# Kernel tuning notes

Measured on AMD Instinct MI355X. Metric: run time of the kernel, lower is better.

Reference implementation:

```python
import jax, jax.numpy as jnp
import numpy as np

T, B, D, H = 512, 128, 256, 256
SIGMA = 0.01


def setup_inputs() -> dict:
    key = jax.random.key(0)
    ks = jax.random.split(key, 5)
    inputs = jax.random.normal(ks[0], (T, B, D), dtype=jnp.float32)
    W_xh_f = jax.random.normal(ks[1], (D, H), dtype=jnp.float32) * SIGMA
    W_hh_f = jax.random.normal(ks[2], (H, H), dtype=jnp.float32) * SIGMA
    b_h_f = jnp.zeros((H,), dtype=jnp.float32)
    W_xh_b = jax.random.normal(ks[3], (D, H), dtype=jnp.float32) * SIGMA
    W_hh_b = jax.random.normal(ks[4], (H, H), dtype=jnp.float32) * SIGMA
    b_h_b = jnp.zeros((H,), dtype=jnp.float32)
    return {"inputs": inputs, "W_xh_f": W_xh_f, "W_hh_f": W_hh_f, "b_h_f": b_h_f,
            "W_xh_b": W_xh_b, "W_hh_b": W_hh_b, "b_h_b": b_h_b}


def _rnn(inputs, W_xh, W_hh, b_h):
    # inputs: [T, B, D]; returns outputs [T, B, H], final state [B, H]
    h0 = jnp.zeros((inputs.shape[1], W_hh.shape[0]), dtype=inputs.dtype)
    # Precompute input projections for all steps (one big GEMM).
    xW = jnp.einsum('tbd,dh->tbh', inputs, W_xh) + b_h

    def step(h, xw_t):
        h = jnp.tanh(xw_t + h @ W_hh)
        return h, h

    hT, outs = jax.lax.scan(step, h0, xW)
    return outs, hT


def reference(inputs, W_xh_f, W_hh_f, b_h_f, W_xh_b, W_hh_b, b_h_b):
    f_outs, f_H = _rnn(inputs, W_xh_f, W_hh_f, b_h_f)          # forward direction
    b_outs, b_H = _rnn(inputs[::-1], W_xh_b, W_hh_b, b_h_b)    # backward direction
    # align backward outputs with original time order and concat on feature dim
    outputs = jnp.concatenate([f_outs, b_outs[::-1]], axis=-1)  # [T, B, 2H]
    return outputs, f_H, b_H
```

## Files before the change

kernel.cpp:

```cpp
#include <hip/hip_runtime.h>
#include <hip/hip_bf16.h>
#include <stdint.h>


typedef short sh8   __attribute__((ext_vector_type(8)));
typedef float f32x4 __attribute__((ext_vector_type(4)));

#define TT 512
#define BB 128
#define HH 256
#define LDH 264

__device__ __forceinline__ unsigned short f2bf(float x) {
    union { float f; unsigned u; } v; v.f = x;
    unsigned r = v.u + 0x7FFFu + ((v.u >> 16) & 1u);
    return (unsigned short)(r >> 16);
}
__device__ __forceinline__ unsigned pk2bf(float lo, float hi) {
    union { __hip_bfloat162 b; unsigned u; } c;
    c.b = __float22bfloat162_rn(make_float2(lo, hi));
    return c.u;
}
__device__ __forceinline__ float tanh5(float x) {
    float e = __builtin_amdgcn_exp2f(x * 2.8853900817779268f);
    return __builtin_fmaf(-2.0f, __builtin_amdgcn_rcpf(e + 1.0f), 1.0f);
}
__device__ __forceinline__ void bar_lds() {
    asm volatile("s_waitcnt lgkmcnt(0)\n\ts_barrier" ::: "memory");
}
__device__ __forceinline__ sh8 pack8(float4 a, float4 b) {
    union { sh8 s; unsigned u[4]; } c;
    c.u[0] = pk2bf(a.x, a.y); c.u[1] = pk2bf(a.z, a.w);
    c.u[2] = pk2bf(b.x, b.y); c.u[3] = pk2bf(b.z, b.w);
    return c.s;
}

__global__ __launch_bounds__(512, 2) void xw_precompute(
    const float* __restrict__ x,
    const float* __restrict__ Wxf, const float* __restrict__ bhf,
    const float* __restrict__ Wxb, const float* __restrict__ bhb,
    float* __restrict__ out)
{
    __shared__ __align__(16) unsigned short xb[2][16 * LDH];

    const int tid = threadIdx.x;
    const int w  = tid >> 6, l = tid & 63;
    const int li = l & 15, lq = l >> 4;
    const int N0 = w * 32;
    const int r0 = blockIdx.x * 256;

    sh8 wf[2][2][8];
#pragma unroll
    for (int d = 0; d < 2; ++d) {
        const float* W = d ? Wxb : Wxf;
#pragma unroll
        for (int nt = 0; nt < 2; ++nt)
#pragma unroll
            for (int kf = 0; kf < 8; ++kf) {
                sh8 t;
#pragma unroll
                for (int j = 0; j < 8; ++j)
                    t[j] = (short)f2bf(W[(size_t)(kf * 32 + lq * 8 + j) * HH + N0 + nt * 16 + li]);
                wf[d][nt][kf] = t;
            }
    }
    f32x4 bias4[2][2];
#pragma unroll
    for (int d = 0; d < 2; ++d) {
        const float* bs = d ? bhb : bhf;
#pragma unroll
        for (int nt = 0; nt < 2; ++nt)
            bias4[d][nt] = *(const f32x4*)&bs[N0 + nt * 16 + lq * 4];
    }

    const int sm = tid >> 5;
    const int sk = (tid & 31) * 8;
    const float* xrow = x + (size_t)(r0 + sm) * HH + sk;

    {
        float4 v0 = *(const float4*)xrow;
        float4 v1 = *(const float4*)(xrow + 4);
        *(sh8*)&xb[0][sm * LDH + sk] = pack8(v0, v1);
    }
    float4 xg0 = *(const float4*)(xrow + 16 * HH);
    float4 xg1 = *(const float4*)(xrow + 16 * HH + 4);
    bar_lds();

    float* obase = out + (size_t)(r0 + li) * 512 + N0 + lq * 4;

    for (int t = 0; t < 16; ++t) {
        const int cur = t & 1, nxt = cur ^ 1;
        {
            *(sh8*)&xb[nxt][sm * LDH + sk] = pack8(xg0, xg1);
            const int t2 = (t + 2 < 16) ? t + 2 : t;
            const float* p = xrow + (size_t)t2 * (16 * HH);
            xg0 = *(const float4*)p;
            xg1 = *(const float4*)(p + 4);
        }
        sh8 xf[8];
#pragma unroll
        for (int kf = 0; kf < 8; ++kf)
            xf[kf] = *(const sh8*)&xb[cur][li * LDH + kf * 32 + lq * 8];

        f32x4 acc[2][2];
#pragma unroll
        for (int d = 0; d < 2; ++d)
#pragma unroll
            for (int nt = 0; nt < 2; ++nt)
                acc[d][nt] = __builtin_amdgcn_mfma_f32_16x16x32_bf16(
                    wf[d][nt][0], xf[0], bias4[d][nt], 0, 0, 0);
#pragma unroll
        for (int kf = 1; kf < 8; ++kf)
#pragma unroll
            for (int d = 0; d < 2; ++d)
#pragma unroll
                for (int nt = 0; nt < 2; ++nt)
                    acc[d][nt] = __builtin_amdgcn_mfma_f32_16x16x32_bf16(
                        wf[d][nt][kf], xf[kf], acc[d][nt], 0, 0, 0);

        float* op = obase + (size_t)t * (16 * 512);
#pragma unroll
        for (int d = 0; d < 2; ++d)
#pragma unroll
            for (int nt = 0; nt < 2; ++nt)
                *(f32x4*)(op + d * HH + nt * 16) = acc[d][nt];
        bar_lds();
    }
}

__global__ __launch_bounds__(512, 2) void rnn_recur(
    const float* __restrict__ Whf, const float* __restrict__ Whb,
    float* __restrict__ out)
{
    __shared__ __align__(16) unsigned short hb[2][16 * LDH];

    const int tid = threadIdx.x;
    const int w  = tid >> 6, l = tid & 63;
    const int li = l & 15, lq = l >> 4;
    const int dir   = blockIdx.x >> 3;
    const int bbase = (blockIdx.x & 7) * 16;
    const float* Wh = dir ? Whb : Whf;
    const int N0 = w * 32;

    sh8 wfh[2][8];
#pragma unroll
    for (int nt = 0; nt < 2; ++nt)
#pragma unroll
        for (int kf = 0; kf < 8; ++kf) {
            sh8 t;
#pragma unroll
            for (int j = 0; j < 8; ++j)
                t[j] = (short)f2bf(Wh[(size_t)(kf * 32 + lq * 8 + j) * HH + N0 + nt * 16 + li]);
            wfh[nt][kf] = t;
        }

    for (int i = tid; i < 16 * LDH / 2; i += 512) ((unsigned*)hb[0])[i] = 0u;

    const ptrdiff_t ostep = dir ? -(ptrdiff_t)(BB * 512) : (ptrdiff_t)(BB * 512);
    const int t0 = dir ? TT - 1 : 0;
    float* op = out + (size_t)t0 * (BB * 512)
                    + (size_t)(bbase + li) * 512 + dir * HH + N0 + lq * 4;
    const float* pf = op + 4 * ostep;
    float* fsp = out + (size_t)TT * BB * 512 + (size_t)dir * (BB * HH)
                     + (size_t)(bbase + li) * HH + N0 + lq * 4;

    f32x4 xA[2], xB[2], xC[2], xD[2];
#pragma unroll
    for (int nt = 0; nt < 2; ++nt) {
        xA[nt] = *(const f32x4*)(op + 0 * ostep + nt * 16);
        xB[nt] = *(const f32x4*)(op + 1 * ostep + nt * 16);
        xC[nt] = *(const f32x4*)(op + 2 * ostep + nt * 16);
        xD[nt] = *(const f32x4*)(op + 3 * ostep + nt * 16);
    }
    const f32x4 zero4 = (f32x4){0.f, 0.f, 0.f, 0.f};

    const unsigned short* hr0 = &hb[0][li * LDH + lq * 8];
    const unsigned short* hr1 = &hb[1][li * LDH + lq * 8];
    unsigned short*       hw0 = &hb[0][li * LDH + N0 + lq * 4];
    unsigned short*       hw1 = &hb[1][li * LDH + N0 + lq * 4];

    bar_lds();

#define STEP(s_, HR, HW, XU)                                                    \
    do {                                                                        \
        sh8 hf[8];                                                              \
        _Pragma("unroll")                                                       \
        for (int kf = 0; kf < 8; ++kf)                                          \
            hf[kf] = *(const sh8*)(HR + kf * 32);                               \
        f32x4 acc[2], acd[2];                                                   \
        __builtin_amdgcn_s_setprio(1);                                          \
        _Pragma("unroll")                                                       \
        for (int nt = 0; nt < 2; ++nt) {         \
            acc[nt] = __builtin_amdgcn_mfma_f32_16x16x32_bf16(                  \
                wfh[nt][0], hf[0], XU[nt], 0, 0, 0);                            \
            acd[nt] = __builtin_amdgcn_mfma_f32_16x16x32_bf16(                  \
                wfh[nt][4], hf[4], zero4, 0, 0, 0);                             \
        }                                                                       \
        _Pragma("unroll")                                                       \
        for (int nt = 0; nt < 2; ++nt)              \
            XU[nt] = *(const f32x4*)(pf + nt * 16);                             \
        pf += ((s_) + 5 < TT) ? ostep : 0;           \
        _Pragma("unroll")                                                       \
        for (int kf = 1; kf < 4; ++kf)                                          \
            _Pragma("unroll")                                                   \
            for (int nt = 0; nt < 2; ++nt) {                                    \
                acc[nt] = __builtin_amdgcn_mfma_f32_16x16x32_bf16(              \
                    wfh[nt][kf], hf[kf], acc[nt], 0, 0, 0);                     \
                acd[nt] = __builtin_amdgcn_mfma_f32_16x16x32_bf16(              \
                    wfh[nt][kf + 4], hf[kf + 4], acd[nt], 0, 0, 0);             \
            }                                                                   \
        __builtin_amdgcn_s_setprio(0);                                          \
        f32x4 vv[2];                                                            \
        _Pragma("unroll")                                                       \
        for (int nt = 0; nt < 2; ++nt) {                                        \
            f32x4 v;                                                            \
            v[0] = tanh5(acc[nt][0] + acd[nt][0]);                              \
            v[1] = tanh5(acc[nt][1] + acd[nt][1]);                              \
            v[2] = tanh5(acc[nt][2] + acd[nt][2]);                              \
            v[3] = tanh5(acc[nt][3] + acd[nt][3]);                              \
            vv[nt] = v;                                                         \
            *(f32x4*)(op + nt * 16) = v;            \
            unsigned plo = pk2bf(v[0], v[1]);                                   \
            unsigned phi = pk2bf(v[2], v[3]);                                   \
            *(uint2*)(HW + nt * 16) = make_uint2(plo, phi);                     \
        }                                                                       \
        if ((s_) == TT - 1) {                                                   \
            _Pragma("unroll")                                                   \
            for (int nt = 0; nt < 2; ++nt)                                      \
                *(f32x4*)(fsp + nt * 16) = vv[nt];                              \
        }                                                                       \
        op += ostep;                                                            \
        bar_lds();                                                              \
    } while (0)

    for (int s = 0; s < TT; s += 4) {
        STEP(s,     hr0, hw1, xA);
        STEP(s + 1, hr1, hw0, xB);
        STEP(s + 2, hr0, hw1, xC);
        STEP(s + 3, hr1, hw0, xD);
    }
#undef STEP
}

extern "C" void kernel_launch(void* const* d_in, const int* in_sizes, int n_in,
                              void* d_out, int out_size, void* d_ws, size_t ws_size,
                              hipStream_t stream)
{
    const float* x   = (const float*)d_in[0];
    const float* Wxf = (const float*)d_in[1];
    const float* Whf = (const float*)d_in[2];
    const float* bhf = (const float*)d_in[3];
    const float* Wxb = (const float*)d_in[4];
    const float* Whb = (const float*)d_in[5];
    const float* bhb = (const float*)d_in[6];

    hipLaunchKernelGGL(xw_precompute, dim3(256), dim3(512), 0, stream,
                       x, Wxf, bhf, Wxb, bhb, (float*)d_out);
    hipLaunchKernelGGL(rnn_recur, dim3(16), dim3(512), 0, stream,
                       Whf, Whb, (float*)d_out);
}
```

Measured before the change: 633.8 us.

## Stage input projections in a workspace with a per-block contiguous permuted layout

When a workspace is large enough, the precompute kernel writes the input projections into a separate buffer laid out so that each recurrence block's per-step slice is contiguous: each lane's 16-byte chunks sit next to its neighbours'. The recurrent kernel then prefetches its per-step input from that buffer with fully coalesced loads instead of strided reads from the output tensor. This is meant to cut the latency of the per-step prefetch on the serial critical path. The cost is an extra workspace buffer, and the code falls back to the old path if no workspace is given.

```diff
diff --git a/kernel.cpp b/kernel.cpp
--- a/kernel.cpp
+++ b/kernel.cpp
@@ -39,7 +39,7 @@
     const float* __restrict__ x,
     const float* __restrict__ Wxf, const float* __restrict__ bhf,
     const float* __restrict__ Wxb, const float* __restrict__ bhb,
-    float* __restrict__ out)
+    float* __restrict__ out, float* __restrict__ xws, int perm)
 {
     __shared__ __align__(16) unsigned short xb[2][16 * LDH];
 
@@ -87,6 +87,8 @@
     bar_lds();
 
     float* obase = out + (size_t)(r0 + li) * 512 + N0 + lq * 4;
+    float* cp0 = xws + (size_t)(r0 / 16) * 8192 + 0 * 4096 + w * 512 + (size_t)l * 4;
+    float* cp1 = xws + (size_t)(r0 / 16) * 8192 + 1 * 4096 + w * 512 + (size_t)l * 4;
 
     for (int t = 0; t < 16; ++t) {
         const int cur = t & 1, nxt = cur ^ 1;
@@ -118,19 +120,27 @@
                     acc[d][nt] = __builtin_amdgcn_mfma_f32_16x16x32_bf16(
                         wf[d][nt][kf], xf[kf], acc[d][nt], 0, 0, 0);
 
-        float* op = obase + (size_t)t * (16 * 512);
-#pragma unroll
-        for (int d = 0; d < 2; ++d)
-#pragma unroll
-            for (int nt = 0; nt < 2; ++nt)
-                *(f32x4*)(op + d * HH + nt * 16) = acc[d][nt];
+        if (perm) {
+#pragma unroll
+            for (int nt = 0; nt < 2; ++nt) {
+                *(f32x4*)(cp0 + (size_t)t * 8192 + nt * 256) = acc[0][nt];
+                *(f32x4*)(cp1 + (size_t)t * 8192 + nt * 256) = acc[1][nt];
+            }
+        } else {
+            float* op = obase + (size_t)t * (16 * 512);
+#pragma unroll
+            for (int d = 0; d < 2; ++d)
+#pragma unroll
+                for (int nt = 0; nt < 2; ++nt)
+                    *(f32x4*)(op + d * HH + nt * 16) = acc[d][nt];
+        }
         bar_lds();
     }
 }
 
 __global__ __launch_bounds__(512, 2) void rnn_recur(
     const float* __restrict__ Whf, const float* __restrict__ Whb,
-    float* __restrict__ out)
+    float* __restrict__ out, const float* __restrict__ xws, int perm)
 {
     __shared__ __align__(16) unsigned short hb[2][16 * LDH];
 
@@ -138,7 +148,8 @@
     const int w  = tid >> 6, l = tid & 63;
     const int li = l & 15, lq = l >> 4;
     const int dir   = blockIdx.x >> 3;
-    const int bbase = (blockIdx.x & 7) * 16;
+    const int g     = blockIdx.x & 7;
+    const int bbase = g * 16;
     const float* Wh = dir ? Whb : Whf;
     const int N0 = w * 32;
 
@@ -160,18 +171,32 @@
     const int t0 = dir ? TT - 1 : 0;
     float* op = out + (size_t)t0 * (BB * 512)
                     + (size_t)(bbase + li) * 512 + dir * HH + N0 + lq * 4;
-    const float* pf = op + 4 * ostep;
     float* fsp = out + (size_t)TT * BB * 512 + (size_t)dir * (BB * HH)
                      + (size_t)(bbase + li) * HH + N0 + lq * 4;
 
+    const float* pfb;
+    ptrdiff_t pstep;
+    int ntoff;
+    if (perm) {
+        pfb = xws + (size_t)(t0 * 8 + g) * 8192 + (size_t)dir * 4096
+                  + w * 512 + (size_t)l * 4;
+        pstep = dir ? -(ptrdiff_t)65536 : (ptrdiff_t)65536;
+        ntoff = 256;
+    } else {
+        pfb = op;
+        pstep = ostep;
+        ntoff = 16;
+    }
+
     f32x4 xA[2], xB[2], xC[2], xD[2];
 #pragma unroll
     for (int nt = 0; nt < 2; ++nt) {
-        xA[nt] = *(const f32x4*)(op + 0 * ostep + nt * 16);
-        xB[nt] = *(const f32x4*)(op + 1 * ostep + nt * 16);
-        xC[nt] = *(const f32x4*)(op + 2 * ostep + nt * 16);
-        xD[nt] = *(const f32x4*)(op + 3 * ostep + nt * 16);
-    }
+        xA[nt] = *(const f32x4*)(pfb + 0 * pstep + nt * ntoff);
+        xB[nt] = *(const f32x4*)(pfb + 1 * pstep + nt * ntoff);
+        xC[nt] = *(const f32x4*)(pfb + 2 * pstep + nt * ntoff);
+        xD[nt] = *(const f32x4*)(pfb + 3 * pstep + nt * ntoff);
+    }
+    const float* pf = pfb + 4 * pstep;
     const f32x4 zero4 = (f32x4){0.f, 0.f, 0.f, 0.f};
 
     const unsigned short* hr0 = &hb[0][li * LDH + lq * 8];
@@ -198,8 +223,8 @@
         }                                                                       \
         _Pragma("unroll")                                                       \
         for (int nt = 0; nt < 2; ++nt)              \
-            XU[nt] = *(const f32x4*)(pf + nt * 16);                             \
-        pf += ((s_) + 5 < TT) ? ostep : 0;           \
+            XU[nt] = *(const f32x4*)(pf + nt * ntoff);                          \
+        pf += ((s_) + 5 < TT) ? pstep : 0;           \
         _Pragma("unroll")                                                       \
         for (int kf = 1; kf < 4; ++kf)                                          \
             _Pragma("unroll")                                                   \
@@ -219,7 +244,7 @@
             v[2] = tanh5(acc[nt][2] + acd[nt][2]);                              \
             v[3] = tanh5(acc[nt][3] + acd[nt][3]);                              \
             vv[nt] = v;                                                         \
-            *(f32x4*)(op + nt * 16) = v;            \
+            *(f32x4*)(op + nt * 16) = v;                                        \
             unsigned plo = pk2bf(v[0], v[1]);                                   \
             unsigned phi = pk2bf(v[2], v[3]);                                   \
             *(uint2*)(HW + nt * 16) = make_uint2(plo, phi);                     \
@@ -254,8 +279,12 @@
     const float* Whb = (const float*)d_in[5];
     const float* bhb = (const float*)d_in[6];
 
+    const size_t XWBYTES = (size_t)TT * BB * 512 * 4;
+    const int perm = (d_ws != nullptr && ws_size >= XWBYTES) ? 1 : 0;
+    float* xws = perm ? (float*)d_ws : (float*)d_out;
+
     hipLaunchKernelGGL(xw_precompute, dim3(256), dim3(512), 0, stream,
-                       x, Wxf, bhf, Wxb, bhb, (float*)d_out);
+                       x, Wxf, bhf, Wxb, bhb, (float*)d_out, xws, perm);
     hipLaunchKernelGGL(rnn_recur, dim3(16), dim3(512), 0, stream,
-                       Whf, Whb, (float*)d_out);
-}
+                       Whf, Whb, (float*)d_out, xws, perm);
+}
```

Result: faster. 581.9 us (-8.2%).
